# Performance work log

Measured on AMD Instinct MI355X. Metric: run time of the kernel, lower is better.

Reference implementation:

```python
import jax, jax.numpy as jnp
import numpy as np

H = 16
D = 1024
HD = D // H

def setup_inputs() -> dict:
    key = jax.random.key(0)
    ks = jax.random.split(key, 5)
    x = jax.random.normal(ks[0], (2, 2048, D), dtype=jnp.float32)
    w_qkv = jax.random.normal(ks[1], (D, 3 * D), dtype=jnp.float32) / np.sqrt(D)
    b_qkv = jax.random.normal(ks[2], (3 * D,), dtype=jnp.float32) * 0.01
    w_o = jax.random.normal(ks[3], (D, D), dtype=jnp.float32) / np.sqrt(D)
    b_o = jax.random.normal(ks[4], (D,), dtype=jnp.float32) * 0.01
    return {"x": x, "w_qkv": w_qkv, "b_qkv": b_qkv, "w_o": w_o, "b_o": b_o}

def reference(x, w_qkv, b_qkv, w_o, b_o):
    b, s, d = x.shape
    qkv = x @ w_qkv + b_qkv                      # [b, s, 3d]
    q, k, v = jnp.split(qkv, 3, axis=-1)
    q = q.reshape(b, s, H, HD)
    k = k.reshape(b, s, H, HD)
    v = v.reshape(b, s, H, HD)
    scores = jnp.einsum('bqhd,bkhd->bhqk', q, k) / jnp.sqrt(jnp.float32(HD))
    attn = jax.nn.softmax(scores, axis=-1)       # [b, h, s, s]
    out = jnp.einsum('bhqk,bkhd->bqhd', attn, v).reshape(b, s, d)
    return out @ w_o + b_o
```

## Files before the change

kernel.cpp:

```cpp
#include <hip/hip_runtime.h>
#include <hip/hip_bf16.h>

typedef unsigned int u32;
typedef unsigned short u16;
typedef __attribute__((ext_vector_type(8))) short bf16x8;
typedef __attribute__((ext_vector_type(4))) float f32x4;
typedef __attribute__((ext_vector_type(16))) float f32x16;
typedef __attribute__((ext_vector_type(8))) u16 u16x8;
typedef __attribute__((ext_vector_type(2))) u32 u32x2;
typedef __attribute__((ext_vector_type(4))) u32 u32x4;

#define MFMA16(A, B, C) __builtin_amdgcn_mfma_f32_16x16x32_bf16(A, B, C, 0, 0, 0)
#define MFMA32(A, B, C) __builtin_amdgcn_mfma_f32_32x32x16_bf16(A, B, C, 0, 0, 0)

#define C_SCALE 0.1803368801111244f

__device__ __forceinline__ u16 f2bf(float f) {
  __hip_bfloat16 h = __float2bfloat16(f);
  u16 u;
  __builtin_memcpy(&u, &h, 2);
  return u;
}

__device__ __forceinline__ u32 pk2(float a, float b) {
  return (u32)f2bf(a) | ((u32)f2bf(b) << 16);
}

__device__ __forceinline__ float exp2fast(float x) {
#if __has_builtin(__builtin_amdgcn_exp2f)
  return __builtin_amdgcn_exp2f(x);
#else
  return exp2f(x);
#endif
}

__device__ __forceinline__ u32x2 pl32swap(u32 a, u32 b) {
  return __builtin_amdgcn_permlane32_swap(a, b, false, false);
}

__device__ __forceinline__ void g2l16(const void* g, void* l) {
  __builtin_amdgcn_global_load_lds(
      (const __attribute__((address_space(1))) u32*)g,
      (__attribute__((address_space(3))) u32*)l, 16, 0, 0);
}

__device__ __forceinline__ void wtrans_tile(const float* __restrict__ in,
                                            u16* __restrict__ out, int R, int C,
                                            int scale_n, float scale,
                                            int c0, int r0, float (*t)[33]) {
  const int tr = threadIdx.x >> 3, tc = (threadIdx.x & 7) << 2;
  const float4 v = *(const float4*)(in + (size_t)(r0 + tr) * C + c0 + tc);
  t[tr][tc] = v.x; t[tr][tc + 1] = v.y; t[tr][tc + 2] = v.z; t[tr][tc + 3] = v.w;
  __syncthreads();
  const float s = (c0 + tr < scale_n) ? scale : 1.f;
  u32 p0 = pk2(t[tc][tr] * s, t[tc + 1][tr] * s);
  u32 p1 = pk2(t[tc + 2][tr] * s, t[tc + 3][tr] * s);
  u32* dst = (u32*)(out + (size_t)(c0 + tr) * R + r0 + tc);
  dst[0] = p0;
  dst[1] = p1;
}

__global__ __launch_bounds__(256) void prep(
    const float* __restrict__ x, u16* __restrict__ xb,
    const float* __restrict__ w_qkv, u16* __restrict__ wqkvt,
    const float* __restrict__ w_o, u16* __restrict__ wot) {
  __shared__ float t[32][33];
  const int bx = blockIdx.x;
  if (bx < 2048) {
    const int i = bx * 256 + threadIdx.x;
    const float4* p = (const float4*)x + (size_t)i * 2;
    const float4 a = p[0], b = p[1];
    u16x8 o;
    o[0] = f2bf(a.x); o[1] = f2bf(a.y); o[2] = f2bf(a.z); o[3] = f2bf(a.w);
    o[4] = f2bf(b.x); o[5] = f2bf(b.y); o[6] = f2bf(b.z); o[7] = f2bf(b.w);
    *((u16x8*)xb + i) = o;
  } else if (bx < 5120) {
    const int tb = bx - 2048;
    wtrans_tile(w_qkv, wqkvt, 1024, 3072, 1024, C_SCALE,
                (tb % 96) << 5, (tb / 96) << 5, t);
  } else {
    const int tb = bx - 5120;
    wtrans_tile(w_o, wot, 1024, 1024, 0, 1.f,
                (tb % 32) << 5, (tb / 32) << 5, t);
  }
}

template <int BN, int OUT_BF16>
__global__ __launch_bounds__(256) void gemm_mfma(
    const u16* __restrict__ A, const u16* __restrict__ Bt,
    const float* __restrict__ bias, void* __restrict__ Cv, int N, int K,
    int bsn, float bsc) {
  constexpr int NI = BN / 32;
  __shared__ u16 As[128 * 32];
  __shared__ u16 Bs[BN * 32];
  const int tid = threadIdx.x;
  const int l = tid & 63, g = l >> 4, lr = l & 15;
  const int w = tid >> 6;
  const int wm = (w >> 1) << 6, wn = (w & 1) * (BN / 2);
  const int bm = blockIdx.y << 7, bn = blockIdx.x * BN;

  f32x4 acc[4][NI];
  const f32x4 zero = {0.f, 0.f, 0.f, 0.f};
#pragma unroll
  for (int i = 0; i < 4; ++i)
#pragma unroll
    for (int j = 0; j < NI; ++j) acc[i][j] = zero;

  const int bi0 = tid, bi1 = 256 + tid;
  const int r0 = bi0 >> 2, lb0 = (bi0 & 3) ^ ((r0 >> 1) & 3);
  const int r1 = bi1 >> 2, lb1 = (bi1 & 3) ^ ((r1 >> 1) & 3);
  const u16* a0 = A + (size_t)(bm + r0) * K + lb0 * 8;
  const u16* a1 = A + (size_t)(bm + r1) * K + lb1 * 8;
  const u16* b0 = Bt + (size_t)(bn + r0) * K + lb0 * 8;
  const u16* b1 = Bt + (size_t)(bn + r1) * K + lb1 * 8;

  const int swA = (lr >> 1) & 3;
  const int aoff = (wm + lr) * 64 + ((g ^ swA) << 4);
  const int boff = (wn + lr) * 64 + ((g ^ swA) << 4);

  for (int k0 = 0; k0 < K; k0 += 32) {
    __syncthreads();
    g2l16(a0 + k0, (char*)As + bi0 * 16);
    g2l16(a1 + k0, (char*)As + bi1 * 16);
    g2l16(b0 + k0, (char*)Bs + bi0 * 16);
    if constexpr (BN == 128) g2l16(b1 + k0, (char*)Bs + bi1 * 16);
    __syncthreads();
    bf16x8 af[4], bfv[NI];
#pragma unroll
    for (int mi = 0; mi < 4; ++mi)
      af[mi] = *(const bf16x8*)((const char*)As + aoff + mi * 1024);
#pragma unroll
    for (int ni = 0; ni < NI; ++ni)
      bfv[ni] = *(const bf16x8*)((const char*)Bs + boff + ni * 1024);
#pragma unroll
    for (int mi = 0; mi < 4; ++mi)
#pragma unroll
      for (int ni = 0; ni < NI; ++ni)
        acc[mi][ni] = MFMA16(af[mi], bfv[ni], acc[mi][ni]);
  }

  float bv[NI];
#pragma unroll
  for (int ni = 0; ni < NI; ++ni) {
    const int col = bn + wn + ni * 16 + lr;
    bv[ni] = bias[col] * (col < bsn ? bsc : 1.f);
  }
  const int crow = bm + wm + (g << 2);
  const int ccol = bn + wn + lr;
  if (OUT_BF16) {
    u16* C = (u16*)Cv;
#pragma unroll
    for (int mi = 0; mi < 4; ++mi)
#pragma unroll
      for (int ni = 0; ni < NI; ++ni)
#pragma unroll
        for (int j = 0; j < 4; ++j)
          C[(size_t)(crow + mi * 16 + j) * N + ccol + ni * 16] =
              f2bf(acc[mi][ni][j] + bv[ni]);
  } else {
    float* C = (float*)Cv;
#pragma unroll
    for (int mi = 0; mi < 4; ++mi)
#pragma unroll
      for (int ni = 0; ni < NI; ++ni)
#pragma unroll
        for (int j = 0; j < 4; ++j)
          C[(size_t)(crow + mi * 16 + j) * N + ccol + ni * 16] =
              acc[mi][ni][j] + bv[ni];
  }
}

__global__ __launch_bounds__(256) void vtrans(const u16* __restrict__ qkvb,
                                              u16* __restrict__ vt) {
  const int wid = (blockIdx.x << 2) + (threadIdx.x >> 6);
  const int l = threadIdx.x & 63;
  const int dc = wid & 7, st = (wid >> 3) & 31, h = (wid >> 8) & 15, b = wid >> 12;
  const int s = (st << 6) + l;
  const u16x8 v = *(const u16x8*)(qkvb + (size_t)(b * 2048 + s) * 3072 + 2048 + h * 64 + dc * 8);
  u16* dst = vt + ((size_t)(((b << 4) + h) << 6) + (dc << 3)) * 2048 + s;
#pragma unroll
  for (int j = 0; j < 8; ++j) dst[(size_t)j * 2048] = v[j];
}

__global__ __launch_bounds__(256, 2) void attn_mfma(
    const u16* __restrict__ qkvb, const u16* __restrict__ vt,
    u16* __restrict__ attnb) {
  __shared__ u16 Qs[128 * 64];
  __shared__ u16 Ks2[2][64 * 64];
  __shared__ u16 Vs2[2][64 * 64];

  const int qt = blockIdx.x, head = blockIdx.y, b = blockIdx.z;
  const int tid = threadIdx.x, w = tid >> 6, l = tid & 63;
  const int lq = l & 31, hw = l >> 5;
  const size_t sb = (size_t)b * 2048;
  const f32x16 z16 = {};

  const int bi0 = tid, bi1 = 256 + tid;
  const int sr0 = bi0 >> 3, slb0 = (bi0 & 7) ^ (sr0 & 7);
  const int sr1 = bi1 >> 3, slb1 = (bi1 & 7) ^ (sr1 & 7);

  const u16* kbase = qkvb + sb * 3072 + 1024 + head * 64;
  const u16* vbase = vt + ((size_t)((b << 4) + head) << 6) * 2048;

  const u16* kp0 = kbase + (size_t)sr0 * 3072 + slb0 * 8;
  const u16* kp1 = kbase + (size_t)sr1 * 3072 + slb1 * 8;
  const u16* vp0 = vbase + (size_t)sr0 * 2048 + slb0 * 8;
  const u16* vp1 = vbase + (size_t)sr1 * 2048 + slb1 * 8;

  {
    const u16* qb = qkvb + (sb + (size_t)qt * 128) * 3072 + head * 64;
#pragma unroll
    for (int j = 0; j < 4; ++j) {
      const int qi = tid + 256 * j;
      const int r = qi >> 3, blk = (qi & 7) ^ (r & 7);
      g2l16(qb + (size_t)r * 3072 + blk * 8, (char*)Qs + qi * 16);
    }
  }
  __syncthreads();

  bf16x8 qf[4];
  {
    const int row = (w << 5) + lq;
#pragma unroll
    for (int dc = 0; dc < 4; ++dc)
      qf[dc] = *(const bf16x8*)((const char*)Qs + row * 128 +
                                (((2 * dc + hw) ^ (row & 7)) << 4));
  }

  float m_run = -1e30f, l_run = 0.f;
  f32x16 o0 = z16, o1 = z16;
  const int xsw = lq & 7;

  for (int kt = 0; kt < 16; ++kt) {
    const size_t ko = (size_t)kt << 7;
    __syncthreads();
    g2l16(kp0 + ko * 3072, (char*)Ks2[0] + bi0 * 16);
    g2l16(kp1 + ko * 3072, (char*)Ks2[0] + bi1 * 16);
    g2l16(kp0 + (ko + 64) * 3072, (char*)Ks2[1] + bi0 * 16);
    g2l16(kp1 + (ko + 64) * 3072, (char*)Ks2[1] + bi1 * 16);
    g2l16(vp0 + ko, (char*)Vs2[0] + bi0 * 16);
    g2l16(vp1 + ko, (char*)Vs2[0] + bi1 * 16);
    g2l16(vp0 + ko + 64, (char*)Vs2[1] + bi0 * 16);
    g2l16(vp1 + ko + 64, (char*)Vs2[1] + bi1 * 16);
    __syncthreads();

    const char* K0 = (const char*)Ks2[0];
    const char* K1 = (const char*)Ks2[1];
    const char* V0 = (const char*)Vs2[0];
    const char* V1 = (const char*)Vs2[1];

    f32x16 s00 = z16, s01 = z16, s10 = z16, s11 = z16;
#pragma unroll
    for (int dc = 0; dc < 4; ++dc) {
      const int off = (((2 * dc + hw) ^ xsw) << 4);
      s00 = MFMA32(*(const bf16x8*)(K0 + lq * 128 + off), qf[dc], s00);
      s01 = MFMA32(*(const bf16x8*)(K0 + (32 + lq) * 128 + off), qf[dc], s01);
      s10 = MFMA32(*(const bf16x8*)(K1 + lq * 128 + off), qf[dc], s10);
      s11 = MFMA32(*(const bf16x8*)(K1 + (32 + lq) * 128 + off), qf[dc], s11);
    }

    float mx = s00[0];
#pragma unroll
    for (int i = 1; i < 16; ++i) mx = fmaxf(mx, s00[i]);
#pragma unroll
    for (int i = 0; i < 16; ++i) mx = fmaxf(mx, s01[i]);
#pragma unroll
    for (int i = 0; i < 16; ++i) mx = fmaxf(mx, s10[i]);
#pragma unroll
    for (int i = 0; i < 16; ++i) mx = fmaxf(mx, s11[i]);
    {
      const u32x2 r = pl32swap(__float_as_uint(mx), __float_as_uint(mx));
      mx = fmaxf(__uint_as_float(r.x), __uint_as_float(r.y));
    }
    if (!__all(mx - m_run <= 8.f)) {
      const float m_new = fmaxf(m_run, mx);
      const float resc = exp2fast(m_run - m_new);
      float rs[16];
#pragma unroll
      for (int r = 0; r < 16; ++r)
        rs[r] = __shfl(resc, (r & 3) + 8 * (r >> 2) + 4 * hw);
#pragma unroll
      for (int r = 0; r < 16; ++r) { o0[r] *= rs[r]; o1[r] *= rs[r]; }
      l_run *= resc;
      m_run = m_new;
    }

    float lsum = 0.f;

#pragma unroll
    for (int i = 0; i < 16; ++i) { s00[i] = exp2fast(s00[i] - m_run); lsum += s00[i]; }
#pragma unroll
    for (int i = 0; i < 16; ++i) { s01[i] = exp2fast(s01[i] - m_run); lsum += s01[i]; }
    bf16x8 pa[4];
#pragma unroll
    for (int kc = 0; kc < 4; ++kc) {
      const f32x16 s = (kc < 2) ? s00 : s01;
      const int q0 = (kc & 1) * 8;
      const u32x2 rA = pl32swap(pk2(s[q0 + 0], s[q0 + 1]), pk2(s[q0 + 4], s[q0 + 5]));
      const u32x2 rB = pl32swap(pk2(s[q0 + 2], s[q0 + 3]), pk2(s[q0 + 6], s[q0 + 7]));
      const u32x4 wds = {rA.x, rB.x, rA.y, rB.y};
      pa[kc] = __builtin_bit_cast(bf16x8, wds);
    }
#pragma unroll
    for (int kc = 0; kc < 4; ++kc) {
      const int off = (((2 * kc + hw) ^ xsw) << 4);
      o0 = MFMA32(pa[kc], *(const bf16x8*)(V0 + lq * 128 + off), o0);
      o1 = MFMA32(pa[kc], *(const bf16x8*)(V0 + (32 + lq) * 128 + off), o1);
    }

#pragma unroll
    for (int i = 0; i < 16; ++i) { s10[i] = exp2fast(s10[i] - m_run); lsum += s10[i]; }
#pragma unroll
    for (int i = 0; i < 16; ++i) { s11[i] = exp2fast(s11[i] - m_run); lsum += s11[i]; }
    bf16x8 pb[4];
#pragma unroll
    for (int kc = 0; kc < 4; ++kc) {
      const f32x16 s = (kc < 2) ? s10 : s11;
      const int q0 = (kc & 1) * 8;
      const u32x2 rA = pl32swap(pk2(s[q0 + 0], s[q0 + 1]), pk2(s[q0 + 4], s[q0 + 5]));
      const u32x2 rB = pl32swap(pk2(s[q0 + 2], s[q0 + 3]), pk2(s[q0 + 6], s[q0 + 7]));
      const u32x4 wds = {rA.x, rB.x, rA.y, rB.y};
      pb[kc] = __builtin_bit_cast(bf16x8, wds);
    }
#pragma unroll
    for (int kc = 0; kc < 4; ++kc) {
      const int off = (((2 * kc + hw) ^ xsw) << 4);
      o0 = MFMA32(pb[kc], *(const bf16x8*)(V1 + lq * 128 + off), o0);
      o1 = MFMA32(pb[kc], *(const bf16x8*)(V1 + (32 + lq) * 128 + off), o1);
    }

    l_run += lsum;
  }

  {
    const u32x2 r = pl32swap(__float_as_uint(l_run), __float_as_uint(l_run));
    l_run = __uint_as_float(r.x) + __uint_as_float(r.y);
  }
  const float invl = 1.f / l_run;
  u16* ob = attnb + (sb + (size_t)qt * 128 + (w << 5)) * 1024 + head * 64;
#pragma unroll
  for (int r = 0; r < 16; ++r) {
    const int qo = (r & 3) + 8 * (r >> 2) + 4 * hw;
    const float iv = __shfl(invl, qo);
    ob[(size_t)qo * 1024 + lq] = f2bf(o0[r] * iv);
    ob[(size_t)qo * 1024 + 32 + lq] = f2bf(o1[r] * iv);
  }
}

extern "C" void kernel_launch(void* const* d_in, const int* in_sizes, int n_in,
                              void* d_out, int out_size, void* d_ws, size_t ws_size,
                              hipStream_t stream) {
  const float* x     = (const float*)d_in[0];
  const float* w_qkv = (const float*)d_in[1];
  const float* b_qkv = (const float*)d_in[2];
  const float* w_o   = (const float*)d_in[3];
  const float* b_o   = (const float*)d_in[4];
  float* out = (float*)d_out;

  u16* xb    = (u16*)d_ws;
  u16* wqkvt = xb + (size_t)4096 * 1024;
  u16* wot   = wqkvt + (size_t)3072 * 1024;
  u16* qkvb  = wot + (size_t)1024 * 1024;
  u16* vtb   = qkvb + (size_t)4096 * 3072;
  u16* attnb = vtb + (size_t)2 * 16 * 64 * 2048;

  prep<<<dim3(6144), dim3(256), 0, stream>>>(x, xb, w_qkv, wqkvt, w_o, wot);

  gemm_mfma<128, 1><<<dim3(24, 32), dim3(256), 0, stream>>>(
      xb, wqkvt, b_qkv, qkvb, 3072, 1024, 1024, C_SCALE);

  vtrans<<<dim3(2048), dim3(256), 0, stream>>>(qkvb, vtb);
  attn_mfma<<<dim3(16, 16, 2), dim3(256), 0, stream>>>(qkvb, vtb, attnb);

  gemm_mfma<64, 0><<<dim3(16, 32), dim3(256), 0, stream>>>(
      attnb, wot, b_o, out, 1024, 1024, 0, 1.f);
}
```

Before: 130.0 us.

## Split attention over KV halves with separate combine kernel

Splits the attention key/value sequence into two halves, launching twice as many blocks. Each block writes unnormalized bf16 partial outputs plus running max and sum, and a new combine kernel merges them with a log-sum-exp rescale. Q is now loaded straight from global memory into registers instead of staged through LDS, which frees shared memory and allows a higher occupancy hint. The gain comes from filling more compute units, paid for with extra partial-result traffic, an additional launch, and one more bf16 rounding of the partial outputs.

```diff
diff --git a/kernel.cpp b/kernel.cpp
--- a/kernel.cpp
+++ b/kernel.cpp
@@ -182,14 +182,14 @@
   for (int j = 0; j < 8; ++j) dst[(size_t)j * 2048] = v[j];
 }
 
-__global__ __launch_bounds__(256, 2) void attn_mfma(
+__global__ __launch_bounds__(256, 4) void attn_split(
     const u16* __restrict__ qkvb, const u16* __restrict__ vt,
-    u16* __restrict__ attnb) {
-  __shared__ u16 Qs[128 * 64];
+    u16* __restrict__ po, float2* __restrict__ ml) {
   __shared__ u16 Ks2[2][64 * 64];
   __shared__ u16 Vs2[2][64 * 64];
 
-  const int qt = blockIdx.x, head = blockIdx.y, b = blockIdx.z;
+  const int qt = blockIdx.x, head = blockIdx.y, z = blockIdx.z;
+  const int b = z >> 1, kc = z & 1;
   const int tid = threadIdx.x, w = tid >> 6, l = tid & 63;
   const int lq = l & 31, hw = l >> 5;
   const size_t sb = (size_t)b * 2048;
@@ -199,39 +199,27 @@
   const int sr0 = bi0 >> 3, slb0 = (bi0 & 7) ^ (sr0 & 7);
   const int sr1 = bi1 >> 3, slb1 = (bi1 & 7) ^ (sr1 & 7);
 
-  const u16* kbase = qkvb + sb * 3072 + 1024 + head * 64;
-  const u16* vbase = vt + ((size_t)((b << 4) + head) << 6) * 2048;
+  const u16* kbase = qkvb + (sb + (size_t)kc * 1024) * 3072 + 1024 + head * 64;
+  const u16* vbase = vt + ((size_t)((b << 4) + head) << 6) * 2048 + (size_t)kc * 1024;
 
   const u16* kp0 = kbase + (size_t)sr0 * 3072 + slb0 * 8;
   const u16* kp1 = kbase + (size_t)sr1 * 3072 + slb1 * 8;
   const u16* vp0 = vbase + (size_t)sr0 * 2048 + slb0 * 8;
   const u16* vp1 = vbase + (size_t)sr1 * 2048 + slb1 * 8;
 
-  {
-    const u16* qb = qkvb + (sb + (size_t)qt * 128) * 3072 + head * 64;
-#pragma unroll
-    for (int j = 0; j < 4; ++j) {
-      const int qi = tid + 256 * j;
-      const int r = qi >> 3, blk = (qi & 7) ^ (r & 7);
-      g2l16(qb + (size_t)r * 3072 + blk * 8, (char*)Qs + qi * 16);
-    }
-  }
-  __syncthreads();
-
   bf16x8 qf[4];
   {
-    const int row = (w << 5) + lq;
-#pragma unroll
-    for (int dc = 0; dc < 4; ++dc)
-      qf[dc] = *(const bf16x8*)((const char*)Qs + row * 128 +
-                                (((2 * dc + hw) ^ (row & 7)) << 4));
+    const u16* qr = qkvb + (sb + (size_t)qt * 128 + (w << 5) + lq) * 3072 +
+                    head * 64 + hw * 8;
+#pragma unroll
+    for (int dc = 0; dc < 4; ++dc) qf[dc] = *(const bf16x8*)(qr + dc * 16);
   }
 
   float m_run = -1e30f, l_run = 0.f;
   f32x16 o0 = z16, o1 = z16;
   const int xsw = lq & 7;
 
-  for (int kt = 0; kt < 16; ++kt) {
+  for (int kt = 0; kt < 8; ++kt) {
     const size_t ko = (size_t)kt << 7;
     __syncthreads();
     g2l16(kp0 + ko * 3072, (char*)Ks2[0] + bi0 * 16);
@@ -293,19 +281,19 @@
     for (int i = 0; i < 16; ++i) { s01[i] = exp2fast(s01[i] - m_run); lsum += s01[i]; }
     bf16x8 pa[4];
 #pragma unroll
-    for (int kc = 0; kc < 4; ++kc) {
-      const f32x16 s = (kc < 2) ? s00 : s01;
-      const int q0 = (kc & 1) * 8;
+    for (int kc2 = 0; kc2 < 4; ++kc2) {
+      const f32x16 s = (kc2 < 2) ? s00 : s01;
+      const int q0 = (kc2 & 1) * 8;
       const u32x2 rA = pl32swap(pk2(s[q0 + 0], s[q0 + 1]), pk2(s[q0 + 4], s[q0 + 5]));
       const u32x2 rB = pl32swap(pk2(s[q0 + 2], s[q0 + 3]), pk2(s[q0 + 6], s[q0 + 7]));
       const u32x4 wds = {rA.x, rB.x, rA.y, rB.y};
-      pa[kc] = __builtin_bit_cast(bf16x8, wds);
-    }
-#pragma unroll
-    for (int kc = 0; kc < 4; ++kc) {
-      const int off = (((2 * kc + hw) ^ xsw) << 4);
-      o0 = MFMA32(pa[kc], *(const bf16x8*)(V0 + lq * 128 + off), o0);
-      o1 = MFMA32(pa[kc], *(const bf16x8*)(V0 + (32 + lq) * 128 + off), o1);
+      pa[kc2] = __builtin_bit_cast(bf16x8, wds);
+    }
+#pragma unroll
+    for (int kc2 = 0; kc2 < 4; ++kc2) {
+      const int off = (((2 * kc2 + hw) ^ xsw) << 4);
+      o0 = MFMA32(pa[kc2], *(const bf16x8*)(V0 + lq * 128 + off), o0);
+      o1 = MFMA32(pa[kc2], *(const bf16x8*)(V0 + (32 + lq) * 128 + off), o1);
     }
 
 #pragma unroll
@@ -314,19 +302,19 @@
     for (int i = 0; i < 16; ++i) { s11[i] = exp2fast(s11[i] - m_run); lsum += s11[i]; }
     bf16x8 pb[4];
 #pragma unroll
-    for (int kc = 0; kc < 4; ++kc) {
-      const f32x16 s = (kc < 2) ? s10 : s11;
-      const int q0 = (kc & 1) * 8;
+    for (int kc2 = 0; kc2 < 4; ++kc2) {
+      const f32x16 s = (kc2 < 2) ? s10 : s11;
+      const int q0 = (kc2 & 1) * 8;
       const u32x2 rA = pl32swap(pk2(s[q0 + 0], s[q0 + 1]), pk2(s[q0 + 4], s[q0 + 5]));
       const u32x2 rB = pl32swap(pk2(s[q0 + 2], s[q0 + 3]), pk2(s[q0 + 6], s[q0 + 7]));
       const u32x4 wds = {rA.x, rB.x, rA.y, rB.y};
-      pb[kc] = __builtin_bit_cast(bf16x8, wds);
-    }
-#pragma unroll
-    for (int kc = 0; kc < 4; ++kc) {
-      const int off = (((2 * kc + hw) ^ xsw) << 4);
-      o0 = MFMA32(pb[kc], *(const bf16x8*)(V1 + lq * 128 + off), o0);
-      o1 = MFMA32(pb[kc], *(const bf16x8*)(V1 + (32 + lq) * 128 + off), o1);
+      pb[kc2] = __builtin_bit_cast(bf16x8, wds);
+    }
+#pragma unroll
+    for (int kc2 = 0; kc2 < 4; ++kc2) {
+      const int off = (((2 * kc2 + hw) ^ xsw) << 4);
+      o0 = MFMA32(pb[kc2], *(const bf16x8*)(V1 + lq * 128 + off), o0);
+      o1 = MFMA32(pb[kc2], *(const bf16x8*)(V1 + (32 + lq) * 128 + off), o1);
     }
 
     l_run += lsum;
@@ -336,14 +324,46 @@
     const u32x2 r = pl32swap(__float_as_uint(l_run), __float_as_uint(l_run));
     l_run = __uint_as_float(r.x) + __uint_as_float(r.y);
   }
-  const float invl = 1.f / l_run;
-  u16* ob = attnb + (sb + (size_t)qt * 128 + (w << 5)) * 1024 + head * 64;
+  const int pid = (z * 16 + head) * 16 + qt;
+  u16* pb2 = po + (size_t)pid * 8192 + (size_t)(w << 5) * 64;
 #pragma unroll
   for (int r = 0; r < 16; ++r) {
     const int qo = (r & 3) + 8 * (r >> 2) + 4 * hw;
-    const float iv = __shfl(invl, qo);
-    ob[(size_t)qo * 1024 + lq] = f2bf(o0[r] * iv);
-    ob[(size_t)qo * 1024 + 32 + lq] = f2bf(o1[r] * iv);
+    pb2[qo * 64 + lq] = f2bf(o0[r]);
+    pb2[qo * 64 + 32 + lq] = f2bf(o1[r]);
+  }
+  if (hw == 0) ml[pid * 128 + (w << 5) + lq] = make_float2(m_run, l_run);
+}
+
+__global__ __launch_bounds__(256) void attn_combine(
+    const u16* __restrict__ po, const float2* __restrict__ ml,
+    u16* __restrict__ attnb) {
+  const int qt = blockIdx.x, head = blockIdx.y, b = blockIdx.z;
+  const int tid = threadIdx.x;
+  const int row = tid >> 1, half = tid & 1;
+  const int pid0 = ((b << 1) * 16 + head) * 16 + qt;
+  const int pid1 = pid0 + 256;
+  const float2 ml0 = ml[pid0 * 128 + row];
+  const float2 ml1 = ml[pid1 * 128 + row];
+  const float m = fmaxf(ml0.x, ml1.x);
+  const float a0 = exp2fast(ml0.x - m), a1 = exp2fast(ml1.x - m);
+  const float inv = 1.f / (ml0.y * a0 + ml1.y * a1);
+  const float s0 = a0 * inv, s1 = a1 * inv;
+  const u16* p0 = po + (size_t)pid0 * 8192 + row * 64 + half * 32;
+  const u16* p1 = po + (size_t)pid1 * 8192 + row * 64 + half * 32;
+  u16* dst = attnb + ((size_t)b * 2048 + (size_t)qt * 128 + row) * 1024 +
+             head * 64 + half * 32;
+#pragma unroll
+  for (int c8 = 0; c8 < 4; ++c8) {
+    const u16x8 v0 = *(const u16x8*)(p0 + c8 * 8);
+    const u16x8 v1 = *(const u16x8*)(p1 + c8 * 8);
+    u16x8 o;
+#pragma unroll
+    for (int j = 0; j < 8; ++j) {
+      const u32 b0 = (u32)(u16)v0[j] << 16, b1 = (u32)(u16)v1[j] << 16;
+      o[j] = f2bf(__uint_as_float(b0) * s0 + __uint_as_float(b1) * s1);
+    }
+    *(u16x8*)(dst + c8 * 8) = o;
   }
 }
 
@@ -363,6 +383,8 @@
   u16* qkvb  = wot + (size_t)1024 * 1024;
   u16* vtb   = qkvb + (size_t)4096 * 3072;
   u16* attnb = vtb + (size_t)2 * 16 * 64 * 2048;
+  u16* pob   = attnb + (size_t)4096 * 1024;
+  float2* mlb = (float2*)(pob + (size_t)1024 * 8192);
 
   prep<<<dim3(6144), dim3(256), 0, stream>>>(x, xb, w_qkv, wqkvt, w_o, wot);
 
@@ -370,7 +392,9 @@
       xb, wqkvt, b_qkv, qkvb, 3072, 1024, 1024, C_SCALE);
 
   vtrans<<<dim3(2048), dim3(256), 0, stream>>>(qkvb, vtb);
-  attn_mfma<<<dim3(16, 16, 2), dim3(256), 0, stream>>>(qkvb, vtb, attnb);
+
+  attn_split<<<dim3(16, 16, 4), dim3(256), 0, stream>>>(qkvb, vtb, pob, mlb);
+  attn_combine<<<dim3(16, 16, 2), dim3(256), 0, stream>>>(pob, mlb, attnb);
 
   gemm_mfma<64, 0><<<dim3(16, 32), dim3(256), 0, stream>>>(
       attnb, wot, b_o, out, 1024, 1024, 0, 1.f);
```

Result: slower. 194.5 us (+49.6%).
